# Kernel tuning notes

Measured on AMD Instinct MI355X. Metric: run time of the kernel, lower is better.

The kernel has to match this reference:

```python
import jax, jax.numpy as jnp
import numpy as np

N = 40000
E = 640000
D_IN = 128
D_H = 128
D_OUT = 1


def setup_inputs() -> dict:
    key = jax.random.key(0)
    ks = jax.random.split(key, 10)
    s = 1.0 / np.sqrt(D_IN)
    sh = 1.0 / np.sqrt(D_H)
    return {
        "x": jax.random.normal(ks[0], (N, D_IN), dtype=jnp.float32),
        "edge_index": jax.random.randint(ks[1], (2, E), 0, N, dtype=jnp.int64),
        # conv1: lin_l (neighbors, has bias), lin_r (root, no bias)
        "W1l": jax.random.uniform(ks[2], (D_IN, D_H), jnp.float32, -s, s),
        "b1": jnp.zeros((D_H,), jnp.float32),
        "W1r": jax.random.uniform(ks[3], (D_IN, D_H), jnp.float32, -s, s),
        # conv2
        "W2l": jax.random.uniform(ks[4], (D_H, D_H), jnp.float32, -sh, sh),
        "b2": jnp.zeros((D_H,), jnp.float32),
        "W2r": jax.random.uniform(ks[5], (D_H, D_H), jnp.float32, -sh, sh),
        # final linear
        "Wo": jax.random.uniform(ks[6], (D_H, D_OUT), jnp.float32, -sh, sh),
        "bo": jnp.zeros((D_OUT,), jnp.float32),
    }


def _mean_aggregate(x, src, dst, num_nodes):
    # mean over incoming edges per target node (PyG SAGEConv default aggr='mean')
    msg_sum = jax.ops.segment_sum(x[src], dst, num_segments=num_nodes)  # [N, D]
    deg = jax.ops.segment_sum(jnp.ones((src.shape[0],), x.dtype), dst,
                              num_segments=num_nodes)
    return msg_sum / jnp.maximum(deg, 1.0)[:, None]


def _sage_conv(x, src, dst, Wl, b, Wr):
    # out = lin_l(mean_agg(neighbors)) + lin_r(x)
    agg = _mean_aggregate(x, src, dst, x.shape[0])
    return agg @ Wl + b + x @ Wr


def reference(x, edge_index, W1l, b1, W1r, W2l, b2, W2r, Wo, bo):
    src, dst = edge_index[0], edge_index[1]
    h = jax.nn.relu(_sage_conv(x, src, dst, W1l, b1, W1r))
    h = jax.nn.relu(_sage_conv(h, src, dst, W2l, b2, W2r))
    return h @ Wo + bo
```

## Files before the change

kernel.cpp:

```cpp
#include <hip/hip_runtime.h>
#include <hip/hip_bf16.h>


#define DH 128
#define CAP 64
#define BCAP 160

typedef __attribute__((ext_vector_type(8))) short bf16x8;
typedef __attribute__((ext_vector_type(4))) float f32x4;

__device__ __forceinline__ unsigned short f2bf_rne(float f) {
    unsigned int u = __float_as_uint(f);
    return (unsigned short)((u + 0x7FFFu + ((u >> 16) & 1u)) >> 16);
}
__device__ __forceinline__ float bf2f(unsigned short h) {
    return __uint_as_float(((unsigned int)h) << 16);
}
__device__ __forceinline__ float bflo(unsigned int u) {
    return __uint_as_float(u << 16);
}
__device__ __forceinline__ float bfhi(unsigned int u) {
    return __uint_as_float(u & 0xffff0000u);
}
__device__ __forceinline__ unsigned packpair_hi(float a, float b) {
    return (__float_as_uint(b) & 0xffff0000u) | (__float_as_uint(a) >> 16);
}
__device__ __forceinline__ unsigned packpair_lo(float a, float b) {
    float ra = a - bfhi(__float_as_uint(a));
    float rb = b - bfhi(__float_as_uint(b));
    return ((unsigned)f2bf_rne(rb) << 16) | f2bf_rne(ra);
}


__global__ __launch_bounds__(256) void prep_kernel(
    const float* __restrict__ x,
    unsigned short* __restrict__ xhi, unsigned short* __restrict__ xlo,
    const int* __restrict__ src, const int* __restrict__ dst,
    int* __restrict__ bcur, unsigned* __restrict__ buckets,
    const float* __restrict__ W1l, const float* __restrict__ W1r,
    const float* __restrict__ W2l, const float* __restrict__ W2r,
    unsigned short* __restrict__ whi, unsigned short* __restrict__ wlo,
    int n4, int E, int nbA, int nbB, int nRanges)
{
    int b = blockIdx.x;
    if (b < nbB) {
        int e = b * 256 + threadIdx.x;
        if (e >= E) return;
        unsigned xcc;
        asm volatile("s_getreg_b32 %0, hwreg(HW_REG_XCC_ID)" : "=s"(xcc));
        xcc &= 7;
        int d = dst[e];
        int s = src[e];
        int range = d >> 5;
        int pos = atomicAdd(&bcur[(int)xcc * nRanges + range], 1);
        if (pos < BCAP)
            buckets[((size_t)range * 8 + xcc) * BCAP + pos] =
                ((unsigned)(d & 31) << 16) | (unsigned)s;
    } else if (b < nbB + nbA) {
        int i = (b - nbB) * 256 + threadIdx.x;
        if (i >= n4) return;
        float4 v = ((const float4*)x)[i];
        unsigned short hx = f2bf_rne(v.x), hy = f2bf_rne(v.y);
        unsigned short hz = f2bf_rne(v.z), hw = f2bf_rne(v.w);
        uint2 hi, lo;
        hi.x = ((unsigned)hy << 16) | hx;
        hi.y = ((unsigned)hw << 16) | hz;
        lo.x = ((unsigned)f2bf_rne(v.y - bf2f(hy)) << 16) | f2bf_rne(v.x - bf2f(hx));
        lo.y = ((unsigned)f2bf_rne(v.w - bf2f(hw)) << 16) | f2bf_rne(v.z - bf2f(hz));
        ((uint2*)xhi)[i] = hi;
        ((uint2*)xlo)[i] = lo;
    } else {
        int tid = (b - nbB - nbA) * 256 + threadIdx.x;
        if (tid >= 2 * 8 * 8 * 64) return;
        int lane = tid & 63;
        int f = (tid >> 6) & 7;
        int t = (tid >> 9) & 7;
        int conv = tid >> 12;
        const float* Wl = conv ? W2l : W1l;
        const float* Wr = conv ? W2r : W1r;
        int c = f * 16 + (lane & 15);
        int kb = t * 32 + (lane >> 4) * 8;
        size_t off = (size_t)tid * 8;
        #pragma unroll
        for (int j = 0; j < 8; ++j) {
            int k = kb + j;
            float w = (k < 128) ? Wl[k * 128 + c] : Wr[(k - 128) * 128 + c];
            unsigned short h = f2bf_rne(w);
            whi[off + j] = h;
            wlo[off + j] = f2bf_rne(w - bf2f(h));
        }
    }
}


__global__ __launch_bounds__(256) void demux_kernel(
    const unsigned* __restrict__ buckets, const int* __restrict__ bcur,
    unsigned short* __restrict__ csr, int* __restrict__ deg, int nRanges)
{
    __shared__ int cnt[32];
    const int b = blockIdx.x;
    const int tid = threadIdx.x;
    if (tid < 32) cnt[tid] = 0;
    __syncthreads();
    const int node0 = b * 32;
    #pragma unroll
    for (int s = 0; s < 8; ++s) {
        int c = min(bcur[s * nRanges + b], BCAP);
        const unsigned* bp = buckets + ((size_t)b * 8 + s) * BCAP;
        for (int i = tid; i < c; i += 256) {
            unsigned p = bp[i];
            int dlow = p >> 16;
            int pos = atomicAdd(&cnt[dlow], 1);
            if (pos < CAP)
                csr[(size_t)(node0 + dlow) * CAP + pos] = (unsigned short)(p & 0xffffu);
        }
    }
    __syncthreads();
    if (tid < 32) deg[node0 + tid] = min(cnt[tid], CAP);
}


__global__ __launch_bounds__(256) void gather_mean_kernel(
    const unsigned short* __restrict__ featbf, const unsigned short* __restrict__ csr,
    const int* __restrict__ deg,
    unsigned short* __restrict__ outhi, unsigned short* __restrict__ outlo, int N)
{
    int node = blockIdx.x * 4 + (threadIdx.x >> 6);
    if (node >= N) return;
    const int lane = threadIdx.x & 63;
    const int ch = lane & 7;
    const int slot = lane >> 3;

    const int dg = min(deg[node], CAP);
    const unsigned short* row = csr + (size_t)node * CAP;

    float a[16], b[16];
    #pragma unroll
    for (int i = 0; i < 16; ++i) { a[i] = 0.f; b[i] = 0.f; }

    int e = slot;
    for (; e + 8 < dg; e += 16) {
        int s0 = row[e];
        int s1 = row[e + 8];
        const uint4* p0 = (const uint4*)&featbf[(size_t)s0 * DH + ch * 16];
        const uint4* p1 = (const uint4*)&featbf[(size_t)s1 * DH + ch * 16];
        uint4 v0 = p0[0], w0 = p0[1];
        uint4 v1 = p1[0], w1 = p1[1];
        a[0] += bflo(v0.x); a[1] += bfhi(v0.x); a[2] += bflo(v0.y); a[3] += bfhi(v0.y);
        a[4] += bflo(v0.z); a[5] += bfhi(v0.z); a[6] += bflo(v0.w); a[7] += bfhi(v0.w);
        a[8] += bflo(w0.x); a[9] += bfhi(w0.x); a[10]+= bflo(w0.y); a[11]+= bfhi(w0.y);
        a[12]+= bflo(w0.z); a[13]+= bfhi(w0.z); a[14]+= bflo(w0.w); a[15]+= bfhi(w0.w);
        b[0] += bflo(v1.x); b[1] += bfhi(v1.x); b[2] += bflo(v1.y); b[3] += bfhi(v1.y);
        b[4] += bflo(v1.z); b[5] += bfhi(v1.z); b[6] += bflo(v1.w); b[7] += bfhi(v1.w);
        b[8] += bflo(w1.x); b[9] += bfhi(w1.x); b[10]+= bflo(w1.y); b[11]+= bfhi(w1.y);
        b[12]+= bflo(w1.z); b[13]+= bfhi(w1.z); b[14]+= bflo(w1.w); b[15]+= bfhi(w1.w);
    }
    if (e < dg) {
        int s0 = row[e];
        const uint4* p0 = (const uint4*)&featbf[(size_t)s0 * DH + ch * 16];
        uint4 v0 = p0[0], w0 = p0[1];
        a[0] += bflo(v0.x); a[1] += bfhi(v0.x); a[2] += bflo(v0.y); a[3] += bfhi(v0.y);
        a[4] += bflo(v0.z); a[5] += bfhi(v0.z); a[6] += bflo(v0.w); a[7] += bfhi(v0.w);
        a[8] += bflo(w0.x); a[9] += bfhi(w0.x); a[10]+= bflo(w0.y); a[11]+= bfhi(w0.y);
        a[12]+= bflo(w0.z); a[13]+= bfhi(w0.z); a[14]+= bflo(w0.w); a[15]+= bfhi(w0.w);
    }
    #pragma unroll
    for (int i = 0; i < 16; ++i) a[i] += b[i];
    #pragma unroll
    for (int m = 8; m < 64; m <<= 1)
        #pragma unroll
        for (int i = 0; i < 16; ++i)
            a[i] += __shfl_xor(a[i], m);

    if (slot == 0) {
        float sc = 1.0f / (float)max(dg, 1);
        #pragma unroll
        for (int i = 0; i < 16; ++i) a[i] *= sc;
        uint4 hi0, hi1, lo0, lo1;
        hi0.x = packpair_hi(a[0], a[1]);   lo0.x = packpair_lo(a[0], a[1]);
        hi0.y = packpair_hi(a[2], a[3]);   lo0.y = packpair_lo(a[2], a[3]);
        hi0.z = packpair_hi(a[4], a[5]);   lo0.z = packpair_lo(a[4], a[5]);
        hi0.w = packpair_hi(a[6], a[7]);   lo0.w = packpair_lo(a[6], a[7]);
        hi1.x = packpair_hi(a[8], a[9]);   lo1.x = packpair_lo(a[8], a[9]);
        hi1.y = packpair_hi(a[10], a[11]); lo1.y = packpair_lo(a[10], a[11]);
        hi1.z = packpair_hi(a[12], a[13]); lo1.z = packpair_lo(a[12], a[13]);
        hi1.w = packpair_hi(a[14], a[15]); lo1.w = packpair_lo(a[14], a[15]);
        uint4* ph = (uint4*)&outhi[(size_t)node * DH + ch * 16];
        uint4* pl = (uint4*)&outlo[(size_t)node * DH + ch * 16];
        ph[0] = hi0; ph[1] = hi1;
        pl[0] = lo0; pl[1] = lo1;
    }
}


template<int HEAD>
__global__ __launch_bounds__(256) void sage_mfma_kernel(
    const unsigned short* __restrict__ agghi, const unsigned short* __restrict__ agglo,
    const unsigned short* __restrict__ xhi, const unsigned short* __restrict__ xlo,
    const unsigned short* __restrict__ whi, const unsigned short* __restrict__ wlo,
    const float* __restrict__ bias,
    unsigned short* __restrict__ Hhi, unsigned short* __restrict__ Hlo,
    const float* __restrict__ Wo, const float* __restrict__ bo,
    float* __restrict__ outp, int N)
{
    const int l = threadIdx.x & 63;
    const int wv = threadIdx.x >> 6;
    const int r = l & 15;
    const int kq = l >> 4;
    const int base0 = blockIdx.x * 128 + wv * 16;
    const int base1 = base0 + 64;
    const bool v1 = (base1 + 16 <= N);

    f32x4 acc0[8], acc1[8];
    #pragma unroll
    for (int f = 0; f < 8; ++f) {
        float b = bias[f * 16 + r];
        acc0[f] = (f32x4){b, b, b, b};
        acc1[f] = (f32x4){b, b, b, b};
    }

    #pragma unroll
    for (int t = 0; t < 8; ++t) {
        const unsigned short* Ah = (t < 4) ? agghi : xhi;
        const unsigned short* Al = (t < 4) ? agglo : xlo;
        size_t ao0 = (size_t)(base0 + r) * DH + (t & 3) * 32 + kq * 8;
        bf16x8 a0h = *(const bf16x8*)&Ah[ao0];
        bf16x8 a0l = *(const bf16x8*)&Al[ao0];
        bf16x8 a1h = {0,0,0,0,0,0,0,0};
        bf16x8 a1l = {0,0,0,0,0,0,0,0};
        if (v1) {
            size_t ao1 = ao0 + (size_t)64 * DH;
            a1h = *(const bf16x8*)&Ah[ao1];
            a1l = *(const bf16x8*)&Al[ao1];
        }
        const unsigned short* bh = whi + ((size_t)(t * 8) * 64 + l) * 8;
        const unsigned short* bl = wlo + ((size_t)(t * 8) * 64 + l) * 8;
        #pragma unroll
        for (int f = 0; f < 8; ++f) {
            bf16x8 bhi = *(const bf16x8*)(bh + (size_t)f * 512);
            bf16x8 blo = *(const bf16x8*)(bl + (size_t)f * 512);
            acc0[f] = __builtin_amdgcn_mfma_f32_16x16x32_bf16(a0h, bhi, acc0[f], 0, 0, 0);
            acc0[f] = __builtin_amdgcn_mfma_f32_16x16x32_bf16(a0l, bhi, acc0[f], 0, 0, 0);
            acc0[f] = __builtin_amdgcn_mfma_f32_16x16x32_bf16(a0h, blo, acc0[f], 0, 0, 0);
            acc1[f] = __builtin_amdgcn_mfma_f32_16x16x32_bf16(a1h, bhi, acc1[f], 0, 0, 0);
            acc1[f] = __builtin_amdgcn_mfma_f32_16x16x32_bf16(a1l, bhi, acc1[f], 0, 0, 0);
            acc1[f] = __builtin_amdgcn_mfma_f32_16x16x32_bf16(a1h, blo, acc1[f], 0, 0, 0);
        }
    }

    if (HEAD == 0) {
        #pragma unroll
        for (int rg = 0; rg < 2; ++rg) {
            if (rg == 1 && !v1) break;
            int base = rg ? base1 : base0;
            #pragma unroll
            for (int f = 0; f < 8; ++f) {
                int col = f * 16 + r;
                #pragma unroll
                for (int q = 0; q < 4; ++q) {
                    float v = fmaxf(rg ? acc1[f][q] : acc0[f][q], 0.0f);
                    size_t idx = (size_t)(base + kq * 4 + q) * DH + col;
                    unsigned short h = f2bf_rne(v);
                    Hhi[idx] = h;
                    Hlo[idx] = f2bf_rne(v - bf2f(h));
                }
            }
        }
    } else {
        float wo[8];
        #pragma unroll
        for (int f = 0; f < 8; ++f) wo[f] = Wo[f * 16 + r];
        #pragma unroll
        for (int rg = 0; rg < 2; ++rg) {
            if (rg == 1 && !v1) break;
            int base = rg ? base1 : base0;
            float s[4] = {0.f, 0.f, 0.f, 0.f};
            #pragma unroll
            for (int f = 0; f < 8; ++f)
                #pragma unroll
                for (int q = 0; q < 4; ++q)
                    s[q] += fmaxf(rg ? acc1[f][q] : acc0[f][q], 0.0f) * wo[f];
            #pragma unroll
            for (int m = 1; m < 16; m <<= 1) {
                s[0] += __shfl_xor(s[0], m);
                s[1] += __shfl_xor(s[1], m);
                s[2] += __shfl_xor(s[2], m);
                s[3] += __shfl_xor(s[3], m);
            }
            if (r < 4) outp[base + kq * 4 + r] = s[r] + bo[0];
        }
    }
}

extern "C" void kernel_launch(void* const* d_in, const int* in_sizes, int n_in,
                              void* d_out, int out_size, void* d_ws, size_t ws_size,
                              hipStream_t stream) {
    const float* x   = (const float*)d_in[0];
    const int*   ei  = (const int*)d_in[1];
    const float* W1l = (const float*)d_in[2];
    const float* b1  = (const float*)d_in[3];
    const float* W1r = (const float*)d_in[4];
    const float* W2l = (const float*)d_in[5];
    const float* b2  = (const float*)d_in[6];
    const float* W2r = (const float*)d_in[7];
    const float* Wo  = (const float*)d_in[8];
    const float* bo  = (const float*)d_in[9];
    float* out = (float*)d_out;

    const int N = in_sizes[0] / DH;
    const int E = in_sizes[1] / 2;
    const int* src = ei;
    const int* dst = ei + E;
    const size_t NDH = (size_t)N * DH;
    const int n4 = N * DH / 4;
    const int nbA = (n4 + 255) / 256;
    const int nbB = (E + 255) / 256;
    const int nRanges = N / 32;

    unsigned short* xhi   = (unsigned short*)d_ws;
    unsigned short* xlo   = xhi + NDH;
    unsigned short* h1hi  = xlo + NDH;
    unsigned short* h1lo  = h1hi + NDH;
    unsigned short* agghi = h1lo + NDH;
    unsigned short* agglo = agghi + NDH;
    unsigned short* whi   = agglo + NDH;
    unsigned short* wlo   = whi + 65536;
    int* bcur = (int*)(wlo + 65536);
    int* deg  = bcur + nRanges * 8;
    unsigned* buckets = (unsigned*)(deg + N);
    unsigned short* csr = (unsigned short*)(buckets + (size_t)nRanges * 8 * BCAP);

    hipMemsetAsync(bcur, 0, (size_t)nRanges * 8 * sizeof(int), stream);
    prep_kernel<<<nbA + nbB + 32, 256, 0, stream>>>(
        x, xhi, xlo, src, dst, bcur, buckets,
        W1l, W1r, W2l, W2r, whi, wlo, n4, E, nbA, nbB, nRanges);
    demux_kernel<<<nRanges, 256, 0, stream>>>(buckets, bcur, csr, deg, nRanges);

    const int convGrid = (N + 127) / 128;

    gather_mean_kernel<<<(N + 3) / 4, 256, 0, stream>>>(
        xhi, csr, deg, agghi, agglo, N);
    sage_mfma_kernel<0><<<convGrid, 256, 0, stream>>>(
        agghi, agglo, xhi, xlo, whi, wlo, b1, h1hi, h1lo,
        nullptr, nullptr, nullptr, N);

    gather_mean_kernel<<<(N + 3) / 4, 256, 0, stream>>>(
        h1hi, csr, deg, agghi, agglo, N);
    sage_mfma_kernel<1><<<convGrid, 256, 0, stream>>>(
        agghi, agglo, h1hi, h1lo, whi + 32768, wlo + 32768, b2, nullptr, nullptr,
        Wo, bo, out, N);
}
```

Measured before the change: 238.9 us.

## Fuse bucket demux into gather kernel with LDS-resident CSR and padded counters

```diff
diff --git a/kernel.cpp b/kernel.cpp
--- a/kernel.cpp
+++ b/kernel.cpp
@@ -52,7 +52,7 @@
         int d = dst[e];
         int s = src[e];
         int range = d >> 5;
-        int pos = atomicAdd(&bcur[(int)xcc * nRanges + range], 1);
+        int pos = atomicAdd(&bcur[((int)xcc * nRanges + range) * 16], 1);
         if (pos < BCAP)
             buckets[((size_t)range * 8 + xcc) * BCAP + pos] =
                 ((unsigned)(d & 31) << 16) | (unsigned)s;
@@ -93,102 +93,99 @@
 }
 
 
-__global__ __launch_bounds__(256) void demux_kernel(
+__global__ __launch_bounds__(512) void gather_demux_kernel(
+    const unsigned short* __restrict__ featbf,
     const unsigned* __restrict__ buckets, const int* __restrict__ bcur,
-    unsigned short* __restrict__ csr, int* __restrict__ deg, int nRanges)
+    unsigned short* __restrict__ outhi, unsigned short* __restrict__ outlo,
+    int nRanges)
 {
+    __shared__ unsigned short csr_lds[32 * CAP];
     __shared__ int cnt[32];
-    const int b = blockIdx.x;
+    const int blk = blockIdx.x;
     const int tid = threadIdx.x;
     if (tid < 32) cnt[tid] = 0;
     __syncthreads();
-    const int node0 = b * 32;
     #pragma unroll
     for (int s = 0; s < 8; ++s) {
-        int c = min(bcur[s * nRanges + b], BCAP);
-        const unsigned* bp = buckets + ((size_t)b * 8 + s) * BCAP;
-        for (int i = tid; i < c; i += 256) {
+        int c = min(bcur[(s * nRanges + blk) * 16], BCAP);
+        const unsigned* bp = buckets + ((size_t)blk * 8 + s) * BCAP;
+        for (int i = tid; i < c; i += 512) {
             unsigned p = bp[i];
             int dlow = p >> 16;
             int pos = atomicAdd(&cnt[dlow], 1);
             if (pos < CAP)
-                csr[(size_t)(node0 + dlow) * CAP + pos] = (unsigned short)(p & 0xffffu);
+                csr_lds[dlow * CAP + pos] = (unsigned short)(p & 0xffffu);
         }
     }
     __syncthreads();
-    if (tid < 32) deg[node0 + tid] = min(cnt[tid], CAP);
-}
-
-
-__global__ __launch_bounds__(256) void gather_mean_kernel(
-    const unsigned short* __restrict__ featbf, const unsigned short* __restrict__ csr,
-    const int* __restrict__ deg,
-    unsigned short* __restrict__ outhi, unsigned short* __restrict__ outlo, int N)
-{
-    int node = blockIdx.x * 4 + (threadIdx.x >> 6);
-    if (node >= N) return;
-    const int lane = threadIdx.x & 63;
+
+    const int lane = tid & 63;
+    const int wv = tid >> 6;
     const int ch = lane & 7;
     const int slot = lane >> 3;
 
-    const int dg = min(deg[node], CAP);
-    const unsigned short* row = csr + (size_t)node * CAP;
-
-    float a[16], b[16];
-    #pragma unroll
-    for (int i = 0; i < 16; ++i) { a[i] = 0.f; b[i] = 0.f; }
-
-    int e = slot;
-    for (; e + 8 < dg; e += 16) {
-        int s0 = row[e];
-        int s1 = row[e + 8];
-        const uint4* p0 = (const uint4*)&featbf[(size_t)s0 * DH + ch * 16];
-        const uint4* p1 = (const uint4*)&featbf[(size_t)s1 * DH + ch * 16];
-        uint4 v0 = p0[0], w0 = p0[1];
-        uint4 v1 = p1[0], w1 = p1[1];
-        a[0] += bflo(v0.x); a[1] += bfhi(v0.x); a[2] += bflo(v0.y); a[3] += bfhi(v0.y);
-        a[4] += bflo(v0.z); a[5] += bfhi(v0.z); a[6] += bflo(v0.w); a[7] += bfhi(v0.w);
-        a[8] += bflo(w0.x); a[9] += bfhi(w0.x); a[10]+= bflo(w0.y); a[11]+= bfhi(w0.y);
-        a[12]+= bflo(w0.z); a[13]+= bfhi(w0.z); a[14]+= bflo(w0.w); a[15]+= bfhi(w0.w);
-        b[0] += bflo(v1.x); b[1] += bfhi(v1.x); b[2] += bflo(v1.y); b[3] += bfhi(v1.y);
-        b[4] += bflo(v1.z); b[5] += bfhi(v1.z); b[6] += bflo(v1.w); b[7] += bfhi(v1.w);
-        b[8] += bflo(w1.x); b[9] += bfhi(w1.x); b[10]+= bflo(w1.y); b[11]+= bfhi(w1.y);
-        b[12]+= bflo(w1.z); b[13]+= bfhi(w1.z); b[14]+= bflo(w1.w); b[15]+= bfhi(w1.w);
-    }
-    if (e < dg) {
-        int s0 = row[e];
-        const uint4* p0 = (const uint4*)&featbf[(size_t)s0 * DH + ch * 16];
-        uint4 v0 = p0[0], w0 = p0[1];
-        a[0] += bflo(v0.x); a[1] += bfhi(v0.x); a[2] += bflo(v0.y); a[3] += bfhi(v0.y);
-        a[4] += bflo(v0.z); a[5] += bfhi(v0.z); a[6] += bflo(v0.w); a[7] += bfhi(v0.w);
-        a[8] += bflo(w0.x); a[9] += bfhi(w0.x); a[10]+= bflo(w0.y); a[11]+= bfhi(w0.y);
-        a[12]+= bflo(w0.z); a[13]+= bfhi(w0.z); a[14]+= bflo(w0.w); a[15]+= bfhi(w0.w);
-    }
-    #pragma unroll
-    for (int i = 0; i < 16; ++i) a[i] += b[i];
-    #pragma unroll
-    for (int m = 8; m < 64; m <<= 1)
-        #pragma unroll
-        for (int i = 0; i < 16; ++i)
-            a[i] += __shfl_xor(a[i], m);
-
-    if (slot == 0) {
-        float sc = 1.0f / (float)max(dg, 1);
-        #pragma unroll
-        for (int i = 0; i < 16; ++i) a[i] *= sc;
-        uint4 hi0, hi1, lo0, lo1;
-        hi0.x = packpair_hi(a[0], a[1]);   lo0.x = packpair_lo(a[0], a[1]);
-        hi0.y = packpair_hi(a[2], a[3]);   lo0.y = packpair_lo(a[2], a[3]);
-        hi0.z = packpair_hi(a[4], a[5]);   lo0.z = packpair_lo(a[4], a[5]);
-        hi0.w = packpair_hi(a[6], a[7]);   lo0.w = packpair_lo(a[6], a[7]);
-        hi1.x = packpair_hi(a[8], a[9]);   lo1.x = packpair_lo(a[8], a[9]);
-        hi1.y = packpair_hi(a[10], a[11]); lo1.y = packpair_lo(a[10], a[11]);
-        hi1.z = packpair_hi(a[12], a[13]); lo1.z = packpair_lo(a[12], a[13]);
-        hi1.w = packpair_hi(a[14], a[15]); lo1.w = packpair_lo(a[14], a[15]);
-        uint4* ph = (uint4*)&outhi[(size_t)node * DH + ch * 16];
-        uint4* pl = (uint4*)&outlo[(size_t)node * DH + ch * 16];
-        ph[0] = hi0; ph[1] = hi1;
-        pl[0] = lo0; pl[1] = lo1;
+    for (int i = 0; i < 4; ++i) {
+        const int nlocal = wv * 4 + i;
+        const int node = blk * 32 + nlocal;
+        const int dg = min(cnt[nlocal], CAP);
+        const unsigned short* row = &csr_lds[nlocal * CAP];
+
+        float a[16], b[16];
+        #pragma unroll
+        for (int j = 0; j < 16; ++j) { a[j] = 0.f; b[j] = 0.f; }
+
+        int e = slot;
+        for (; e + 8 < dg; e += 16) {
+            int s0 = row[e];
+            int s1 = row[e + 8];
+            const uint4* p0 = (const uint4*)&featbf[(size_t)s0 * DH + ch * 16];
+            const uint4* p1 = (const uint4*)&featbf[(size_t)s1 * DH + ch * 16];
+            uint4 v0 = p0[0], w0 = p0[1];
+            uint4 v1 = p1[0], w1 = p1[1];
+            a[0] += bflo(v0.x); a[1] += bfhi(v0.x); a[2] += bflo(v0.y); a[3] += bfhi(v0.y);
+            a[4] += bflo(v0.z); a[5] += bfhi(v0.z); a[6] += bflo(v0.w); a[7] += bfhi(v0.w);
+            a[8] += bflo(w0.x); a[9] += bfhi(w0.x); a[10]+= bflo(w0.y); a[11]+= bfhi(w0.y);
+            a[12]+= bflo(w0.z); a[13]+= bfhi(w0.z); a[14]+= bflo(w0.w); a[15]+= bfhi(w0.w);
+            b[0] += bflo(v1.x); b[1] += bfhi(v1.x); b[2] += bflo(v1.y); b[3] += bfhi(v1.y);
+            b[4] += bflo(v1.z); b[5] += bfhi(v1.z); b[6] += bflo(v1.w); b[7] += bfhi(v1.w);
+            b[8] += bflo(w1.x); b[9] += bfhi(w1.x); b[10]+= bflo(w1.y); b[11]+= bfhi(w1.y);
+            b[12]+= bflo(w1.z); b[13]+= bfhi(w1.z); b[14]+= bflo(w1.w); b[15]+= bfhi(w1.w);
+        }
+        if (e < dg) {
+            int s0 = row[e];
+            const uint4* p0 = (const uint4*)&featbf[(size_t)s0 * DH + ch * 16];
+            uint4 v0 = p0[0], w0 = p0[1];
+            a[0] += bflo(v0.x); a[1] += bfhi(v0.x); a[2] += bflo(v0.y); a[3] += bfhi(v0.y);
+            a[4] += bflo(v0.z); a[5] += bfhi(v0.z); a[6] += bflo(v0.w); a[7] += bfhi(v0.w);
+            a[8] += bflo(w0.x); a[9] += bfhi(w0.x); a[10]+= bflo(w0.y); a[11]+= bfhi(w0.y);
+            a[12]+= bflo(w0.z); a[13]+= bfhi(w0.z); a[14]+= bflo(w0.w); a[15]+= bfhi(w0.w);
+        }
+        #pragma unroll
+        for (int j = 0; j < 16; ++j) a[j] += b[j];
+        #pragma unroll
+        for (int m = 8; m < 64; m <<= 1)
+            #pragma unroll
+            for (int j = 0; j < 16; ++j)
+                a[j] += __shfl_xor(a[j], m);
+
+        if (slot == 0) {
+            float sc = 1.0f / (float)max(dg, 1);
+            #pragma unroll
+            for (int j = 0; j < 16; ++j) a[j] *= sc;
+            uint4 hi0, hi1, lo0, lo1;
+            hi0.x = packpair_hi(a[0], a[1]);   lo0.x = packpair_lo(a[0], a[1]);
+            hi0.y = packpair_hi(a[2], a[3]);   lo0.y = packpair_lo(a[2], a[3]);
+            hi0.z = packpair_hi(a[4], a[5]);   lo0.z = packpair_lo(a[4], a[5]);
+            hi0.w = packpair_hi(a[6], a[7]);   lo0.w = packpair_lo(a[6], a[7]);
+            hi1.x = packpair_hi(a[8], a[9]);   lo1.x = packpair_lo(a[8], a[9]);
+            hi1.y = packpair_hi(a[10], a[11]); lo1.y = packpair_lo(a[10], a[11]);
+            hi1.z = packpair_hi(a[12], a[13]); lo1.z = packpair_lo(a[12], a[13]);
+            hi1.w = packpair_hi(a[14], a[15]); lo1.w = packpair_lo(a[14], a[15]);
+            uint4* ph = (uint4*)&outhi[(size_t)node * DH + ch * 16];
+            uint4* pl = (uint4*)&outlo[(size_t)node * DH + ch * 16];
+            ph[0] = hi0; ph[1] = hi1;
+            pl[0] = lo0; pl[1] = lo1;
+        }
     }
 }
 
@@ -326,26 +323,23 @@
     unsigned short* whi   = agglo + NDH;
     unsigned short* wlo   = whi + 65536;
     int* bcur = (int*)(wlo + 65536);
-    int* deg  = bcur + nRanges * 8;
-    unsigned* buckets = (unsigned*)(deg + N);
-    unsigned short* csr = (unsigned short*)(buckets + (size_t)nRanges * 8 * BCAP);
-
-    hipMemsetAsync(bcur, 0, (size_t)nRanges * 8 * sizeof(int), stream);
+    unsigned* buckets = (unsigned*)(bcur + (size_t)nRanges * 8 * 16);
+
+    hipMemsetAsync(bcur, 0, (size_t)nRanges * 8 * 16 * sizeof(int), stream);
     prep_kernel<<<nbA + nbB + 32, 256, 0, stream>>>(
         x, xhi, xlo, src, dst, bcur, buckets,
         W1l, W1r, W2l, W2r, whi, wlo, n4, E, nbA, nbB, nRanges);
-    demux_kernel<<<nRanges, 256, 0, stream>>>(buckets, bcur, csr, deg, nRanges);
 
     const int convGrid = (N + 127) / 128;
 
-    gather_mean_kernel<<<(N + 3) / 4, 256, 0, stream>>>(
-        xhi, csr, deg, agghi, agglo, N);
+    gather_demux_kernel<<<nRanges, 512, 0, stream>>>(
+        xhi, buckets, bcur, agghi, agglo, nRanges);
     sage_mfma_kernel<0><<<convGrid, 256, 0, stream>>>(
         agghi, agglo, xhi, xlo, whi, wlo, b1, h1hi, h1lo,
         nullptr, nullptr, nullptr, N);
 
-    gather_mean_kernel<<<(N + 3) / 4, 256, 0, stream>>>(
-        h1hi, csr, deg, agghi, agglo, N);
+    gather_demux_kernel<<<nRanges, 512, 0, stream>>>(
+        h1hi, buckets, bcur, agghi, agglo, nRanges);
     sage_mfma_kernel<1><<<convGrid, 256, 0, stream>>>(
         agghi, agglo, h1hi, h1lo, whi + 32768, wlo + 32768, b2, nullptr, nullptr,
         Wo, bo, out, N);
```

Result: no change. 237.7 us (-0.5%).
